# Performance work log

Hardware: AMD Instinct MI355X
Metric: run time of the kernel (lower is better)

The kernel has to match this reference:

```python
import jax, jax.numpy as jnp
import numpy as np


def setup_inputs() -> dict:
    key = jax.random.key(0)
    k1, k2, k3 = jax.random.split(key, 3)
    B, C_IN, C_OUT, R, K = 4, 64, 64, 64, 3
    x = jax.random.normal(k1, (B, C_IN, R, R, R), dtype=jnp.float32)
    # per-voxel nonzero test |x|.sum(channel) != 0 used by the module)
    keep = jax.random.uniform(k2, (B, 1, R, R, R)) < 0.3
    x = x * keep.astype(jnp.float32)
    weight = jax.random.normal(k3, (C_OUT, C_IN, K, K, K), dtype=jnp.float32)
    return {"x": x, "weight": weight}


def reference(x, weight):
    # The torch module gathers a k^3 neighborhood at every nonzero input voxel,
    # contracts with the (unflipped) weight, and scatters to the same voxel.
    # This is exactly cross-correlation (torch conv semantics) with SAME padding,
    # masked to voxels where the input is nonzero across channels.
    K = weight.shape[-1]
    pad_l = K // 2
    pad_r = K - 1 - pad_l
    out = jax.lax.conv_general_dilated(
        x, weight,
        window_strides=(1, 1, 1),
        padding=[(pad_l, pad_r)] * 3,
        dimension_numbers=("NCDHW", "OIDHW", "NCDHW"),
    )  # [B, C_out, D, H, W]
    mask = (jnp.abs(x).sum(axis=1, keepdims=True) != 0)  # [B,1,D,H,W]
    return out * mask.astype(out.dtype)
```

## Files before the change

### kernel.cpp

```cpp
#include <hip/hip_runtime.h>
#include <stdint.h>


#define R3 262144
#define NVOX (4 * R3)
#define P  66
#define PS (66 * 66)
#define PB (66 * 66 * 66)
#define WSW_ELEMS (27 * 2 * 4 * 64 * 8)
#define CAP (NVOX / 2)

typedef __attribute__((ext_vector_type(4))) float f32x4;
typedef __attribute__((ext_vector_type(8))) short short8;

static __device__ inline unsigned short f2bf(float f) {
    union { float f; unsigned u; } v; v.f = f;
    unsigned u = v.u;
    return (unsigned short)((u + 0x7fffu + ((u >> 16) & 1u)) >> 16);
}

static __device__ __forceinline__ void gload16(const void* g, void* l) {
    __builtin_amdgcn_global_load_lds(
        (const __attribute__((address_space(1))) unsigned int*)g,
        (__attribute__((address_space(3))) unsigned int*)l, 16, 0, 0);
}

__global__ void wprep(const float* __restrict__ w, unsigned short* __restrict__ wsw) {
    int e = blockIdx.x * 256 + threadIdx.x;
    if (e >= WSW_ELEMS) return;
    int j    = e & 7;
    int lane = (e >> 3) & 63;
    int nt   = (e >> 9) & 3;
    int kc   = (e >> 11) & 1;
    int tap  = e >> 12;
    int co = nt * 16 + (lane & 15);
    int ci = kc * 32 + ((lane >> 4) * 8) + j;
    wsw[e] = f2bf(w[(co * 64 + ci) * 27 + tap]);
}

__global__ void __launch_bounds__(256) halo_zero(uint4* __restrict__ xt4) {
    int p = blockIdx.x * 256 + threadIdx.x;
    if (p >= 4 * PB) return;
    int b = p / PB;
    int rp = p - b * PB;
    int z = rp / PS; rp -= z * PS;
    int y = rp / P;  int xx = rp - y * P;
    if (z == 0 || z == 65 || y == 0 || y == 65 || xx == 0 || xx == 65) {
        uint4 zz = {0, 0, 0, 0};
        uint4* d = xt4 + (size_t)p * 8;
#pragma unroll
        for (int k = 0; k < 8; ++k) d[k] = zz;
    }
}

__global__ void __launch_bounds__(256) xprep(const float* __restrict__ x,
                                             unsigned int* __restrict__ xt_u32,
                                             int* __restrict__ list,
                                             int* __restrict__ pos,
                                             int* __restrict__ count) {
    __shared__ unsigned int lds[256 * 36];
    __shared__ unsigned int wcnt[4], wbase[4], bbase;
    int t = threadIdx.x;
    int v = blockIdx.x * 256 + t;
    int b = v >> 18;
    int s = v & (R3 - 1);
    const float* xb = x + (size_t)b * (64 * R3) + s;
    bool active = false;
    unsigned int pk[32];
#pragma unroll
    for (int c2 = 0; c2 < 32; ++c2) {
        float f0 = xb[(size_t)(2 * c2) * R3];
        float f1 = xb[(size_t)(2 * c2 + 1) * R3];
        active |= (f0 != 0.f) | (f1 != 0.f);
        pk[c2] = (unsigned)f2bf(f0) | ((unsigned)f2bf(f1) << 16);
    }
#pragma unroll
    for (int k = 0; k < 8; ++k) {
        uint4 q = { pk[4 * k], pk[4 * k + 1], pk[4 * k + 2], pk[4 * k + 3] };
        *(uint4*)&lds[t * 36 + 4 * k] = q;
    }
    __syncthreads();
    int s0 = (blockIdx.x * 256) & (R3 - 1);
    int z0 = s0 >> 12;
    int y0 = (s0 >> 6) & 63;
    size_t rowbase = ((size_t)b * PB + (size_t)(z0 + 1) * PS + (size_t)(y0 + 1) * P + 1) * 32;
#pragma unroll
    for (int i = 0; i < 8; ++i) {
        int g4 = i * 256 + t;
        int vox = g4 >> 3;
        int col = (g4 & 7) * 4;
        uint4 val = *(const uint4*)&lds[vox * 36 + col];
        int r = vox >> 6;
        int xc = vox & 63;
        *(uint4*)&xt_u32[rowbase + (size_t)r * (P * 32) + (size_t)xc * 32 + col] = val;
    }
    int lane = t & 63, w = t >> 6;
    unsigned long long bal = __ballot(active);
    if (lane == 0) wcnt[w] = (unsigned)__popcll(bal);
    __syncthreads();
    if (t == 0) {
        unsigned tot = 0;
        for (int i = 0; i < 4; ++i) { wbase[i] = tot; tot += wcnt[i]; }
        bbase = (unsigned)atomicAdd(count, (int)tot);
    }
    __syncthreads();
    int p = -1;
    if (active) {
        unsigned pp = bbase + wbase[w] + (unsigned)__popcll(bal & ((1ULL << lane) - 1ULL));
        list[pp] = v;
        p = (int)pp;
    }
    pos[v] = p;
}

#define STAGE(tap, buf) do {                                                       \
    const int dz_ = (tap) / 9 - 1, dy_ = ((tap) / 3) % 3 - 1, dx_ = (tap) % 3 - 1; \
    const ptrdiff_t dlt_ = (ptrdiff_t)(dz_ * PS + dy_ * P + dx_) * 128;            \
    _Pragma("unroll")                                                              \
    for (int i_ = 0; i_ < 4; ++i_)                                                 \
        gload16(asrc[i_] + dlt_, &Ab[buf][(t + i_ * 256) * 16]);                   \
    _Pragma("unroll")                                                              \
    for (int i_ = 0; i_ < 2; ++i_)                                                 \
        gload16(wswb + (size_t)(tap) * 8192 + (t + i_ * 256) * 16,                 \
                &Bb[buf][(t + i_ * 256) * 16]);                                    \
} while (0)

__global__ void __launch_bounds__(256) sconv_gemm(const unsigned char* __restrict__ xt,
                                                  const unsigned char* __restrict__ wswb,
                                                  const int* __restrict__ list,
                                                  const int* __restrict__ count_p,
                                                  float* __restrict__ out,
                                                  float* __restrict__ compact,
                                                  int use_compact) {
    __shared__ __align__(16) unsigned char Ab[2][16384];
    __shared__ __align__(16) unsigned char Bb[2][8192];
    __shared__ int vids[128];
    int count = *count_p;
    int base = blockIdx.x * 128;
    if (base >= count) return;
    int t = threadIdx.x;
    if (t < 128) { int idx = base + t; vids[t] = (idx < count) ? list[idx] : -1; }
    __syncthreads();

    const unsigned char* asrc[4];
    {
        int seg = t & 7;
        int r0 = t >> 3;
        int off = (seg * 16) ^ ((r0 & 7) << 4);
#pragma unroll
        for (int i = 0; i < 4; ++i) {
            int vid = vids[r0 + 32 * i];
            if (vid < 0) vid = 0;
            int bb = vid >> 18, sp = vid & (R3 - 1);
            int vz = sp >> 12, vy = (sp >> 6) & 63, vx = sp & 63;
            size_t pvox = (size_t)bb * PB + (size_t)(vz + 1) * PS + (size_t)(vy + 1) * P + (vx + 1);
            asrc[i] = xt + pvox * 128 + off;
        }
    }

    int lane = t & 63, w = t >> 6;
    int cl = lane & 15;
    int hi16 = (lane >> 4) * 16;
    int aswz = (cl & 7) << 4;
    int aoff[2][2];
#pragma unroll
    for (int m = 0; m < 2; ++m)
#pragma unroll
        for (int kc = 0; kc < 2; ++kc)
            aoff[m][kc] = (w * 32 + m * 16 + cl) * 128 + ((kc * 64 + hi16) ^ aswz);
    int boff[2][4];
#pragma unroll
    for (int kc = 0; kc < 2; ++kc)
#pragma unroll
        for (int n = 0; n < 4; ++n)
            boff[kc][n] = ((kc * 4 + n) * 64 + lane) * 16;

    f32x4 acc[2][4] = {};

    STAGE(0, 0);
#pragma unroll
    for (int tap = 0; tap < 27; ++tap) {
        const int cur = tap & 1;
        asm volatile("s_waitcnt vmcnt(0)" ::: "memory");
        asm volatile("s_barrier" ::: "memory");
        if (tap < 26) { STAGE(tap + 1, cur ^ 1); }
#pragma unroll
        for (int kc = 0; kc < 2; ++kc) {
            short8 a0 = *(const short8*)&Ab[cur][aoff[0][kc]];
            short8 a1 = *(const short8*)&Ab[cur][aoff[1][kc]];
#pragma unroll
            for (int n = 0; n < 4; ++n) {
                short8 bf = *(const short8*)&Bb[cur][boff[kc][n]];
                acc[0][n] = __builtin_amdgcn_mfma_f32_16x16x32_bf16(a0, bf, acc[0][n], 0, 0, 0);
                acc[1][n] = __builtin_amdgcn_mfma_f32_16x16x32_bf16(a1, bf, acc[1][n], 0, 0, 0);
            }
        }
        asm volatile("s_waitcnt lgkmcnt(0)" ::: "memory");
    }

    int q = lane >> 4;
    if (use_compact) {
#pragma unroll
        for (int m = 0; m < 2; ++m) {
#pragma unroll
            for (int rg = 0; rg < 4; ++rg) {
                int row = w * 32 + m * 16 + q * 4 + rg;
                int gi = base + row;
                if (gi < count && gi < CAP) {
#pragma unroll
                    for (int n = 0; n < 4; ++n)
                        compact[(size_t)gi * 64 + n * 16 + cl] = acc[m][n][rg];
                }
            }
        }
    } else {
#pragma unroll
        for (int m = 0; m < 2; ++m) {
#pragma unroll
            for (int rg = 0; rg < 4; ++rg) {
                int row = w * 32 + m * 16 + q * 4 + rg;
                if (base + row < count) {
                    int vv = vids[row];
                    int bb2 = vv >> 18;
                    int sp = vv & (R3 - 1);
                    float* op = out + (size_t)(bb2 * 64 + cl) * R3 + sp;
#pragma unroll
                    for (int n = 0; n < 4; ++n)
                        op[(size_t)(n * 16) * R3] = acc[m][n][rg];
                }
            }
        }
    }
}

__global__ void __launch_bounds__(256) finalize(const uint4* __restrict__ compact4,
                                                const int* __restrict__ pos,
                                                float* __restrict__ out) {
    __shared__ uint4 rows[256 * 17];
    __shared__ int lpos[256];
    int t = threadIdx.x;
    int vb = blockIdx.x * 256;
    int b = vb >> 18;
    int sp0 = vb & (R3 - 1);
    lpos[t] = pos[vb + t];
    __syncthreads();
#pragma unroll
    for (int it = 0; it < 16; ++it) {
        int item = it * 256 + t;
        int vox = item >> 4, seg = item & 15;
        int q = lpos[vox];
        uint4 val = {0, 0, 0, 0};
        if ((unsigned)q < (unsigned)CAP) val = compact4[(size_t)q * 16 + seg];
        rows[vox * 17 + seg] = val;
    }
    __syncthreads();
    const float* rf = (const float*)rows;
    float* ob = out + (size_t)b * 64 * R3 + sp0 + t;
#pragma unroll
    for (int co = 0; co < 64; ++co)
        ob[(size_t)co * R3] = rf[t * 68 + co];
}

__global__ void __launch_bounds__(64) fallback_conv(const float* __restrict__ x,
                                                    const float* __restrict__ wt,
                                                    float* __restrict__ out) {
    __shared__ float rowb[66];
    int bid = blockIdx.x;
    int y = bid & 63, z = (bid >> 6) & 63, co = (bid >> 12) & 63, b = bid >> 18;
    int t = threadIdx.x;
    float acc = 0.f;
    bool active = false;
    for (int ci = 0; ci < 64; ++ci) {
        const float* xp = x + ((size_t)(b * 64 + ci)) * R3;
        const float* wp = wt + ((size_t)(co * 64 + ci)) * 27;
        for (int dz = -1; dz <= 1; ++dz) {
            int nz = z + dz;
            bool okz = (unsigned)nz < 64u;
            for (int dy = -1; dy <= 1; ++dy) {
                int ny = y + dy;
                bool ok = okz && ((unsigned)ny < 64u);
                float v = ok ? xp[nz * 4096 + ny * 64 + t] : 0.f;
                rowb[t + 1] = v;
                if (t == 0) { rowb[0] = 0.f; rowb[65] = 0.f; }
                __syncthreads();
                if (dz == 0 && dy == 0) active |= (rowb[t + 1] != 0.f);
                const float* wq = wp + (dz + 1) * 9 + (dy + 1) * 3;
                acc += rowb[t] * wq[0] + rowb[t + 1] * wq[1] + rowb[t + 2] * wq[2];
                __syncthreads();
            }
        }
    }
    out[((size_t)(b * 64 + co)) * R3 + z * 4096 + y * 64 + t] = active ? acc : 0.f;
}

extern "C" void kernel_launch(void* const* d_in, const int* in_sizes, int n_in,
                              void* d_out, int out_size, void* d_ws, size_t ws_size,
                              hipStream_t stream) {
    const float* x = (const float*)d_in[0];
    const float* w = (const float*)d_in[1];
    float* out = (float*)d_out;

    const size_t XT_BYTES = (size_t)4 * PB * 128;
    const size_t LIST_OFF = XT_BYTES;
    const size_t POS_OFF  = LIST_OFF + (size_t)NVOX * 4;
    const size_t WSW_OFF  = POS_OFF + (size_t)NVOX * 4;
    const size_t CNT_OFF  = WSW_OFF + (size_t)WSW_ELEMS * 2;
    const size_t CMP_OFF  = (CNT_OFF + 256 + 255) & ~(size_t)255;
    const size_t NEED_S   = CMP_OFF;
    const size_t NEED_C   = CMP_OFF + (size_t)CAP * 64 * 4;

    if (ws_size < NEED_S) {
        fallback_conv<<<NVOX, 64, 0, stream>>>(x, w, out);
        return;
    }

    unsigned int*   xt   = (unsigned int*)d_ws;
    int*            list = (int*)((char*)d_ws + LIST_OFF);
    int*            pos  = (int*)((char*)d_ws + POS_OFF);
    unsigned short* wsw  = (unsigned short*)((char*)d_ws + WSW_OFF);
    int*            cnt  = (int*)((char*)d_ws + CNT_OFF);
    float*          cmp  = (float*)((char*)d_ws + CMP_OFF);
    int use_compact = (ws_size >= NEED_C) ? 1 : 0;

    hipMemsetAsync(cnt, 0, sizeof(int), stream);
    if (!use_compact)
        hipMemsetAsync(d_out, 0, (size_t)out_size * sizeof(float), stream);
    wprep<<<WSW_ELEMS / 256, 256, 0, stream>>>(w, wsw);
    halo_zero<<<(4 * PB + 255) / 256, 256, 0, stream>>>((uint4*)d_ws);
    xprep<<<NVOX / 256, 256, 0, stream>>>(x, xt, list, pos, cnt);
    sconv_gemm<<<NVOX / 128, 256, 0, stream>>>((const unsigned char*)xt,
                                               (const unsigned char*)wsw, list, cnt,
                                               out, cmp, use_compact);
    if (use_compact)
        finalize<<<NVOX / 256, 256, 0, stream>>>((const uint4*)cmp, pos, out);
}
```

Baseline: 686.9 us.

## Triple-buffer tap staging, remap tiles per XCD, register-based finalize transpose

The GEMM kernel moves from double to triple buffering of the A/B LDS tiles, prefetching two taps ahead and waiting with a partial vmcnt so loads overlap compute longer. Block IDs are remapped so consecutive tiles land on the same XCD, aiming for better L2 locality of neighbouring voxel gathers. The finalize kernel drops its LDS transpose and holds each voxel's 64 outputs in registers, removing barriers and shared-memory traffic. In exchange, LDS use rises to about 74KB per block, which may lower occupancy, and finalize's per-thread strided global reads may coalesce worse.

```diff
diff --git a/kernel.cpp b/kernel.cpp
--- a/kernel.cpp
+++ b/kernel.cpp
@@ -132,12 +132,17 @@
                                                   float* __restrict__ out,
                                                   float* __restrict__ compact,
                                                   int use_compact) {
-    __shared__ __align__(16) unsigned char Ab[2][16384];
-    __shared__ __align__(16) unsigned char Bb[2][8192];
+    __shared__ __align__(16) unsigned char Ab[3][16384];
+    __shared__ __align__(16) unsigned char Bb[3][8192];
     __shared__ int vids[128];
     int count = *count_p;
-    int base = blockIdx.x * 128;
-    if (base >= count) return;
+    int nt_act = (count + 127) >> 7;
+    int bid = blockIdx.x;
+    if (bid >= nt_act) return;
+    int qd = nt_act >> 3, rd = nt_act & 7;
+    int xcd = bid & 7, ixx = bid >> 3;
+    int tile = (xcd < rd ? xcd * (qd + 1) : rd * (qd + 1) + (xcd - rd) * qd) + ixx;
+    int base = tile * 128;
     int t = threadIdx.x;
     if (t < 128) { int idx = base + t; vids[t] = (idx < count) ? list[idx] : -1; }
     __syncthreads();
@@ -178,12 +183,14 @@
     f32x4 acc[2][4] = {};
 
     STAGE(0, 0);
+    STAGE(1, 1);
 #pragma unroll
     for (int tap = 0; tap < 27; ++tap) {
-        const int cur = tap & 1;
-        asm volatile("s_waitcnt vmcnt(0)" ::: "memory");
+        const int cur = tap % 3;
+        if (tap < 26) asm volatile("s_waitcnt vmcnt(6)" ::: "memory");
+        else          asm volatile("s_waitcnt vmcnt(0)" ::: "memory");
         asm volatile("s_barrier" ::: "memory");
-        if (tap < 26) { STAGE(tap + 1, cur ^ 1); }
+        if (tap < 25) { STAGE(tap + 2, (tap + 2) % 3); }
 #pragma unroll
         for (int kc = 0; kc < 2; ++kc) {
             short8 a0 = *(const short8*)&Ab[cur][aoff[0][kc]];
@@ -236,29 +243,25 @@
 __global__ void __launch_bounds__(256) finalize(const uint4* __restrict__ compact4,
                                                 const int* __restrict__ pos,
                                                 float* __restrict__ out) {
-    __shared__ uint4 rows[256 * 17];
-    __shared__ int lpos[256];
     int t = threadIdx.x;
     int vb = blockIdx.x * 256;
     int b = vb >> 18;
     int sp0 = vb & (R3 - 1);
-    lpos[t] = pos[vb + t];
-    __syncthreads();
-#pragma unroll
-    for (int it = 0; it < 16; ++it) {
-        int item = it * 256 + t;
-        int vox = item >> 4, seg = item & 15;
-        int q = lpos[vox];
-        uint4 val = {0, 0, 0, 0};
-        if ((unsigned)q < (unsigned)CAP) val = compact4[(size_t)q * 16 + seg];
-        rows[vox * 17 + seg] = val;
-    }
-    __syncthreads();
-    const float* rf = (const float*)rows;
+    int q = pos[vb + t];
+    bool act = (unsigned)q < (unsigned)CAP;
+    const uint4* src = compact4 + (size_t)(act ? q : 0) * 16;
+    uint4 r[16];
+#pragma unroll
+    for (int s = 0; s < 16; ++s) {
+        uint4 v = {0, 0, 0, 0};
+        if (act) v = src[s];
+        r[s] = v;
+    }
+    const float* rf = (const float*)r;
     float* ob = out + (size_t)b * 64 * R3 + sp0 + t;
 #pragma unroll
     for (int co = 0; co < 64; ++co)
-        ob[(size_t)co * R3] = rf[t * 68 + co];
+        ob[(size_t)co * R3] = rf[co];
 }
 
 __global__ void __launch_bounds__(64) fallback_conv(const float* __restrict__ x,
```

New measurement: 656.9 us. 4.4% less time.
